# Kernel tuning notes

Hardware: AMD Instinct MI355X
Metric: run time of the kernel (lower is better)

The kernel has to match this reference:

```python
import jax, jax.numpy as jnp
import numpy as np

ALPHA = 0.2          # LeakyReLU negative slope
NEG_BIG = -9e15      # mask fill value from the original code
N, IN_F, OUT_F = 8192, 128, 64


def setup_inputs() -> dict:
    key = jax.random.key(0)
    k1, k2, k3, k4 = jax.random.split(key, 4)
    h = jax.random.normal(k1, (N, IN_F), dtype=jnp.float32)
    adj = jax.random.randint(k2, (N, N), 0, 2, dtype=jnp.int32)
    W = jax.random.normal(k3, (IN_F, OUT_F), dtype=jnp.float32) * 0.1
    a = jax.random.normal(k4, (2 * OUT_F, 1), dtype=jnp.float32) * 0.1
    return {"h": h, "adj": adj, "W": W, "a": a}


def reference(h, adj, W, a):
    # Wh: [N, F]
    Wh = h @ W
    # e_ij = leakyrelu([Wh_i ; Wh_j] . a) = leakyrelu(Wh_i.a1 + Wh_j.a2)
    # (identical math to the original NxNx2F concat, without materializing it)
    a1 = a[:OUT_F, 0]   # [F]
    a2 = a[OUT_F:, 0]   # [F]
    s1 = Wh @ a1        # [N]
    s2 = Wh @ a2        # [N]
    e = jax.nn.leaky_relu(s1[:, None] + s2[None, :], negative_slope=ALPHA)  # [N, N]
    e = jnp.where(adj > 0, e, jnp.float32(NEG_BIG))
    attention = jax.nn.softmax(e, axis=1)
    # dropout is identity at inference (training=False)
    h_prime = attention @ Wh  # [N, F]
    return jax.nn.elu(h_prime)  # concat=True -> elu
```

## Files before the change

### kernel.cpp

```cpp
#include <hip/hip_runtime.h>
#include <hip/hip_bf16.h>

#define N 8192
#define IN_F 128
#define OUT_F 64
#define LRELU_ALPHA 0.2f
#define CH 1024
#define NIT 8
#define PSTR 1040

typedef __attribute__((ext_vector_type(8))) short short8;
typedef __attribute__((ext_vector_type(4))) float float4v;
typedef __attribute__((ext_vector_type(4))) unsigned short ushortx4;

__device__ __forceinline__ unsigned short bf16_bits(float x) {
  unsigned u = __builtin_bit_cast(unsigned, x);
  u += 0x7fffu + ((u >> 16) & 1u);
  return (unsigned short)(u >> 16);
}

__global__ __launch_bounds__(256) void prep_kernel(
    const float* __restrict__ h, const float* __restrict__ W,
    const float* __restrict__ a, float* __restrict__ s1,
    float* __restrict__ s2, unsigned short* __restrict__ whT) {
  const int tid = threadIdx.x;
  const int row = blockIdx.x * 4 + (tid >> 6);
  const int k = tid & 63;
  const float* hr = h + row * IN_F;
  float acc = 0.f;
#pragma unroll 8
  for (int c = 0; c < IN_F; ++c) acc = fmaf(hr[c], W[c * OUT_F + k], acc);
  whT[(long)k * N + row] = bf16_bits(acc);
  float p1 = acc * a[k];
  float p2 = acc * a[OUT_F + k];
#pragma unroll
  for (int off = 32; off > 0; off >>= 1) {
    p1 += __shfl_xor(p1, off);
    p2 += __shfl_xor(p2, off);
  }
  if (k == 0) { s1[row] = p1; s2[row] = p2; }
}

__global__ __launch_bounds__(256) void repack_kernel(
    const unsigned short* __restrict__ whT, unsigned short* __restrict__ whF) {
  const int f = blockIdx.x * 256 + threadIdx.x;
  const int lane = f & 63, tt = (f >> 6) & 3, c = f >> 8;
  const int r16 = lane & 15, quad = lane >> 4;
  const short8 v = *(const short8*)(whT + (long)(tt * 16 + r16) * N + c * 32 + quad * 8);
  *(short8*)(whF + (long)f * 8) = v;
}

__device__ __forceinline__ void p_write(unsigned short* pr, int c, int4 av,
                                        float4 s2v, float s1w) {
  float e0 = s1w + s2v.x; e0 = fmaxf(e0, LRELU_ALPHA * e0);
  float e1 = s1w + s2v.y; e1 = fmaxf(e1, LRELU_ALPHA * e1);
  float e2 = s1w + s2v.z; e2 = fmaxf(e2, LRELU_ALPHA * e2);
  float e3 = s1w + s2v.w; e3 = fmaxf(e3, LRELU_ALPHA * e3);
  const float p0 = av.x > 0 ? __expf(e0) : 0.f;
  const float p1 = av.y > 0 ? __expf(e1) : 0.f;
  const float p2 = av.z > 0 ? __expf(e2) : 0.f;
  const float p3 = av.w > 0 ? __expf(e3) : 0.f;
  ushortx4 pk = {bf16_bits(p0), bf16_bits(p1), bf16_bits(p2), bf16_bits(p3)};
  *(ushortx4*)(pr + c) = pk;
}

__global__ __launch_bounds__(1024, 4) void gat_kernel(
    const int* __restrict__ adj, const float* __restrict__ s1,
    const float* __restrict__ s2, const unsigned short* __restrict__ whF,
    float* __restrict__ out) {
  __shared__ __align__(16) unsigned short pbuf[2][16][PSTR];
  const int tid = threadIdx.x;
  const int w = tid >> 6, L = tid & 63;
  const int r16 = L & 15, quad = L >> 4;
  const int row0 = blockIdx.x * 16;
  const long arow = (long)(row0 + w) * N;
  const float s1w = s1[row0 + w];

  float4v acc0 = {0.f, 0.f, 0.f, 0.f};
  float4v acc1 = {0.f, 0.f, 0.f, 0.f};
  float4v acc2 = {0.f, 0.f, 0.f, 0.f};
  float4v acc3 = {0.f, 0.f, 0.f, 0.f};
  float4v accD = {0.f, 0.f, 0.f, 0.f};
  const short ONE = (short)0x3F80;
  const short8 ones = {ONE, ONE, ONE, ONE, ONE, ONE, ONE, ONE};

  int4 ra[4];
  float4 rs[4];
#pragma unroll
  for (int k = 0; k < 4; ++k) {
    ra[k] = *(const int4*)(adj + arow + k * 256 + L * 4);
    rs[k] = *(const float4*)(s2 + k * 256 + L * 4);
  }
#pragma unroll
  for (int k = 0; k < 4; ++k)
    p_write(pbuf[0][w], k * 256 + L * 4, ra[k], rs[k], s1w);
#pragma unroll
  for (int k = 0; k < 4; ++k) {
    ra[k] = *(const int4*)(adj + arow + CH + k * 256 + L * 4);
    rs[k] = *(const float4*)(s2 + CH + k * 256 + L * 4);
  }
  __syncthreads();

  for (int it = 0; it < NIT; ++it) {
    const int b = it & 1;
    if (it < NIT - 1) {
      unsigned short* pr = pbuf[b ^ 1][w];
#pragma unroll
      for (int k = 0; k < 4; ++k)
        p_write(pr, k * 256 + L * 4, ra[k], rs[k], s1w);
      if (it < NIT - 2) {
        const long base = arow + (long)(it + 2) * CH + L * 4;
        const int sbase = (it + 2) * CH + L * 4;
#pragma unroll
        for (int k = 0; k < 4; ++k) {
          ra[k] = *(const int4*)(adj + base + k * 256);
          rs[k] = *(const float4*)(s2 + sbase + k * 256);
        }
      }
    }
#pragma unroll
    for (int sub = 0; sub < 2; ++sub) {
      const int lc = (sub * 16 + w) * 32;
      const short8 afrag = *(const short8*)(&pbuf[b][r16][lc + quad * 8]);
      const int c32 = it * 32 + sub * 16 + w;
      const unsigned short* bp = whF + ((long)c32 * 256 + L) * 8;
      const short8 b0 = *(const short8*)(bp);
      const short8 b1 = *(const short8*)(bp + 512);
      const short8 b2 = *(const short8*)(bp + 1024);
      const short8 b3 = *(const short8*)(bp + 1536);
      acc0 = __builtin_amdgcn_mfma_f32_16x16x32_bf16(afrag, b0, acc0, 0, 0, 0);
      acc1 = __builtin_amdgcn_mfma_f32_16x16x32_bf16(afrag, b1, acc1, 0, 0, 0);
      acc2 = __builtin_amdgcn_mfma_f32_16x16x32_bf16(afrag, b2, acc2, 0, 0, 0);
      acc3 = __builtin_amdgcn_mfma_f32_16x16x32_bf16(afrag, b3, acc3, 0, 0, 0);
      accD = __builtin_amdgcn_mfma_f32_16x16x32_bf16(afrag, ones, accD, 0, 0, 0);
    }
    __syncthreads();
  }

  float* M = (float*)pbuf;
  if (w >= 8) {
    float* S = M + (w - 8) * 1040;
#pragma unroll
    for (int reg = 0; reg < 4; ++reg) {
      const int r = quad * 4 + reg;
      S[r * 64 + 0 * 16 + r16] = acc0[reg];
      S[r * 64 + 1 * 16 + r16] = acc1[reg];
      S[r * 64 + 2 * 16 + r16] = acc2[reg];
      S[r * 64 + 3 * 16 + r16] = acc3[reg];
      if (r16 == 0) S[1024 + r] = accD[reg];
    }
  }
  __syncthreads();
  if (w < 8) {
    float* S = M + w * 1040;
#pragma unroll
    for (int reg = 0; reg < 4; ++reg) {
      const int r = quad * 4 + reg;
      S[r * 64 + 0 * 16 + r16] += acc0[reg];
      S[r * 64 + 1 * 16 + r16] += acc1[reg];
      S[r * 64 + 2 * 16 + r16] += acc2[reg];
      S[r * 64 + 3 * 16 + r16] += acc3[reg];
      if (r16 == 0) S[1024 + r] += accD[reg];
    }
  }
  __syncthreads();
  {
    const int r = tid >> 6, k = tid & 63;
    float Sv = 0.f, Lv = 0.f;
#pragma unroll
    for (int s = 0; s < 8; ++s) {
      Sv += M[s * 1040 + r * 64 + k];
      Lv += M[s * 1040 + 1024 + r];
    }
    const float v = Sv / Lv;
    out[(long)(row0 + r) * OUT_F + k] = v > 0.f ? v : expm1f(v);
  }
}

extern "C" void kernel_launch(void* const* d_in, const int* in_sizes, int n_in,
                              void* d_out, int out_size, void* d_ws, size_t ws_size,
                              hipStream_t stream) {
  const float* h = (const float*)d_in[0];
  const int* adj = (const int*)d_in[1];
  const float* W = (const float*)d_in[2];
  const float* a = (const float*)d_in[3];
  float* out = (float*)d_out;

  float* s1 = (float*)d_ws;
  float* s2 = s1 + N;
  unsigned short* whT = (unsigned short*)(s2 + N);
  unsigned short* whF = whT + (long)OUT_F * N;

  prep_kernel<<<N / 4, 256, 0, stream>>>(h, W, a, s1, s2, whT);
  repack_kernel<<<N * OUT_F / 8 / 256, 256, 0, stream>>>(whT, whF);
  gat_kernel<<<N / 16, 1024, 0, stream>>>(adj, s1, s2, whF, out);
}
```

Measured before the change: 397.6 us.

## Split columns across blocks with 64-row tiles and a separate merge kernel

Restructures the attention kernel so each block handles 64 rows and a quarter of the columns (split-K). Each whF B-fragment load is now reused across four row tiles instead of one. The row sum moves from an MFMA against a ones vector to a scalar accumulation plus wave shuffles. Partial numerators and denominators go to workspace, and a new merge kernel sums them and applies normalization and ELU. This cuts redundant global reads of Wh, but adds workspace traffic, an extra launch and higher register pressure from 16 accumulators.

```diff
diff --git a/kernel.cpp b/kernel.cpp
--- a/kernel.cpp
+++ b/kernel.cpp
@@ -5,11 +5,15 @@
 #define IN_F 128
 #define OUT_F 64
 #define LRELU_ALPHA 0.2f
-#define CH 1024
-#define NIT 8
-#define PSTR 1040
+#define SPLIT 4
+#define RPB 64
+#define CPB 2048
+#define WIN 512
+#define NWIN 4
+#define TSTR 129
 
 typedef __attribute__((ext_vector_type(8))) short short8;
+typedef __attribute__((ext_vector_type(4))) short short4v;
 typedef __attribute__((ext_vector_type(4))) float float4v;
 typedef __attribute__((ext_vector_type(4))) unsigned short ushortx4;
 
@@ -50,7 +54,7 @@
   *(short8*)(whF + (long)f * 8) = v;
 }
 
-__device__ __forceinline__ void p_write(unsigned short* pr, int c, int4 av,
+__device__ __forceinline__ float p_half(unsigned short* dst, int4 av,
                                         float4 s2v, float s1w) {
   float e0 = s1w + s2v.x; e0 = fmaxf(e0, LRELU_ALPHA * e0);
   float e1 = s1w + s2v.y; e1 = fmaxf(e1, LRELU_ALPHA * e1);
@@ -61,120 +65,154 @@
   const float p2 = av.z > 0 ? __expf(e2) : 0.f;
   const float p3 = av.w > 0 ? __expf(e3) : 0.f;
   ushortx4 pk = {bf16_bits(p0), bf16_bits(p1), bf16_bits(p2), bf16_bits(p3)};
-  *(ushortx4*)(pr + c) = pk;
-}
-
-__global__ __launch_bounds__(1024, 4) void gat_kernel(
+  *(ushortx4*)dst = pk;
+  return (p0 + p1) + (p2 + p3);
+}
+
+__global__ __launch_bounds__(512, 4) void gat_kernel(
     const int* __restrict__ adj, const float* __restrict__ s1,
     const float* __restrict__ s2, const unsigned short* __restrict__ whF,
-    float* __restrict__ out) {
-  __shared__ __align__(16) unsigned short pbuf[2][16][PSTR];
+    float* __restrict__ pacc, float* __restrict__ pl) {
+  __shared__ __align__(16) unsigned short ptile[RPB * TSTR * 4];
+  __shared__ __align__(16) float s2l[CPB];
   const int tid = threadIdx.x;
   const int w = tid >> 6, L = tid & 63;
   const int r16 = L & 15, quad = L >> 4;
-  const int row0 = blockIdx.x * 16;
-  const long arow = (long)(row0 + w) * N;
-  const float s1w = s1[row0 + w];
-
-  float4v acc0 = {0.f, 0.f, 0.f, 0.f};
-  float4v acc1 = {0.f, 0.f, 0.f, 0.f};
-  float4v acc2 = {0.f, 0.f, 0.f, 0.f};
-  float4v acc3 = {0.f, 0.f, 0.f, 0.f};
-  float4v accD = {0.f, 0.f, 0.f, 0.f};
-  const short ONE = (short)0x3F80;
-  const short8 ones = {ONE, ONE, ONE, ONE, ONE, ONE, ONE, ONE};
-
-  int4 ra[4];
-  float4 rs[4];
-#pragma unroll
-  for (int k = 0; k < 4; ++k) {
-    ra[k] = *(const int4*)(adj + arow + k * 256 + L * 4);
-    rs[k] = *(const float4*)(s2 + k * 256 + L * 4);
-  }
-#pragma unroll
-  for (int k = 0; k < 4; ++k)
-    p_write(pbuf[0][w], k * 256 + L * 4, ra[k], rs[k], s1w);
-#pragma unroll
-  for (int k = 0; k < 4; ++k) {
-    ra[k] = *(const int4*)(adj + arow + CH + k * 256 + L * 4);
-    rs[k] = *(const float4*)(s2 + CH + k * 256 + L * 4);
-  }
+  const int rb = blockIdx.x, cs = blockIdx.y;
+  const int row0 = rb * RPB;
+  const int colbase = cs * CPB;
+
+  *(float4*)(s2l + tid * 4) = *(const float4*)(s2 + colbase + tid * 4);
+
+  float s1r[8];
+#pragma unroll
+  for (int j = 0; j < 8; ++j) s1r[j] = s1[row0 + w * 8 + j];
+
+  float lsum[8] = {0.f, 0.f, 0.f, 0.f, 0.f, 0.f, 0.f, 0.f};
+  float4v acc[4][4];
+#pragma unroll
+  for (int rt = 0; rt < 4; ++rt)
+#pragma unroll
+    for (int dt = 0; dt < 4; ++dt) acc[rt][dt] = (float4v){0.f, 0.f, 0.f, 0.f};
+
   __syncthreads();
 
-  for (int it = 0; it < NIT; ++it) {
-    const int b = it & 1;
-    if (it < NIT - 1) {
-      unsigned short* pr = pbuf[b ^ 1][w];
-#pragma unroll
-      for (int k = 0; k < 4; ++k)
-        p_write(pr, k * 256 + L * 4, ra[k], rs[k], s1w);
-      if (it < NIT - 2) {
-        const long base = arow + (long)(it + 2) * CH + L * 4;
-        const int sbase = (it + 2) * CH + L * 4;
-#pragma unroll
-        for (int k = 0; k < 4; ++k) {
-          ra[k] = *(const int4*)(adj + base + k * 256);
-          rs[k] = *(const float4*)(s2 + sbase + k * 256);
-        }
+  for (int it = 0; it < NWIN; ++it) {
+    const int c0 = it * WIN + L * 4;
+    const float4 sva = *(const float4*)(s2l + c0);
+    const float4 svb = *(const float4*)(s2l + c0 + 256);
+#pragma unroll
+    for (int half = 0; half < 2; ++half) {
+      int4 ja[4], jb[4];
+#pragma unroll
+      for (int j2 = 0; j2 < 4; ++j2) {
+        const int r = half * 4 + j2;
+        const long arow = (long)(row0 + w * 8 + r) * N + colbase + c0;
+        ja[j2] = *(const int4*)(adj + arow);
+        jb[j2] = *(const int4*)(adj + arow + 256);
+      }
+#pragma unroll
+      for (int j2 = 0; j2 < 4; ++j2) {
+        const int r = half * 4 + j2;
+        unsigned short* rowp = ptile + (w * 8 + r) * TSTR * 4;
+        lsum[r] += p_half(rowp + L * 4, ja[j2], sva, s1r[r]);
+        lsum[r] += p_half(rowp + (64 + L) * 4, jb[j2], svb, s1r[r]);
       }
     }
-#pragma unroll
-    for (int sub = 0; sub < 2; ++sub) {
-      const int lc = (sub * 16 + w) * 32;
-      const short8 afrag = *(const short8*)(&pbuf[b][r16][lc + quad * 8]);
-      const int c32 = it * 32 + sub * 16 + w;
-      const unsigned short* bp = whF + ((long)c32 * 256 + L) * 8;
+    __syncthreads();
+#pragma unroll
+    for (int ci = 0; ci < 2; ++ci) {
+      const int c = w + ci * 8;
+      const unsigned short* bp =
+          whF + ((long)(cs * 64 + it * 16 + c) * 256 + L) * 8;
       const short8 b0 = *(const short8*)(bp);
       const short8 b1 = *(const short8*)(bp + 512);
       const short8 b2 = *(const short8*)(bp + 1024);
       const short8 b3 = *(const short8*)(bp + 1536);
-      acc0 = __builtin_amdgcn_mfma_f32_16x16x32_bf16(afrag, b0, acc0, 0, 0, 0);
-      acc1 = __builtin_amdgcn_mfma_f32_16x16x32_bf16(afrag, b1, acc1, 0, 0, 0);
-      acc2 = __builtin_amdgcn_mfma_f32_16x16x32_bf16(afrag, b2, acc2, 0, 0, 0);
-      acc3 = __builtin_amdgcn_mfma_f32_16x16x32_bf16(afrag, b3, acc3, 0, 0, 0);
-      accD = __builtin_amdgcn_mfma_f32_16x16x32_bf16(afrag, ones, accD, 0, 0, 0);
+#pragma unroll
+      for (int rt = 0; rt < 4; ++rt) {
+        const int g = (rt * 16 + r16) * TSTR + c * 8 + quad * 2;
+        const short4v alo = *(const short4v*)(ptile + g * 4);
+        const short4v ahi = *(const short4v*)(ptile + g * 4 + 4);
+        const short8 afrag =
+            __builtin_shufflevector(alo, ahi, 0, 1, 2, 3, 4, 5, 6, 7);
+        acc[rt][0] = __builtin_amdgcn_mfma_f32_16x16x32_bf16(afrag, b0, acc[rt][0], 0, 0, 0);
+        acc[rt][1] = __builtin_amdgcn_mfma_f32_16x16x32_bf16(afrag, b1, acc[rt][1], 0, 0, 0);
+        acc[rt][2] = __builtin_amdgcn_mfma_f32_16x16x32_bf16(afrag, b2, acc[rt][2], 0, 0, 0);
+        acc[rt][3] = __builtin_amdgcn_mfma_f32_16x16x32_bf16(afrag, b3, acc[rt][3], 0, 0, 0);
+      }
     }
     __syncthreads();
   }
 
-  float* M = (float*)pbuf;
-  if (w >= 8) {
-    float* S = M + (w - 8) * 1040;
-#pragma unroll
-    for (int reg = 0; reg < 4; ++reg) {
-      const int r = quad * 4 + reg;
-      S[r * 64 + 0 * 16 + r16] = acc0[reg];
-      S[r * 64 + 1 * 16 + r16] = acc1[reg];
-      S[r * 64 + 2 * 16 + r16] = acc2[reg];
-      S[r * 64 + 3 * 16 + r16] = acc3[reg];
-      if (r16 == 0) S[1024 + r] = accD[reg];
-    }
+#pragma unroll
+  for (int j = 0; j < 8; ++j) {
+    float v = lsum[j];
+#pragma unroll
+    for (int off = 1; off < 64; off <<= 1) v += __shfl_xor(v, off);
+    if (L == 0) pl[(long)cs * N + row0 + w * 8 + j] = v;
+  }
+
+  float* M = (float*)ptile;
+  if (w >= 4) {
+    float* S = M + (w - 4) * 4096;
+#pragma unroll
+    for (int rt = 0; rt < 4; ++rt)
+#pragma unroll
+      for (int dt = 0; dt < 4; ++dt)
+#pragma unroll
+        for (int reg = 0; reg < 4; ++reg)
+          S[(rt * 16 + quad * 4 + reg) * 64 + dt * 16 + r16] = acc[rt][dt][reg];
   }
   __syncthreads();
-  if (w < 8) {
-    float* S = M + w * 1040;
-#pragma unroll
-    for (int reg = 0; reg < 4; ++reg) {
-      const int r = quad * 4 + reg;
-      S[r * 64 + 0 * 16 + r16] += acc0[reg];
-      S[r * 64 + 1 * 16 + r16] += acc1[reg];
-      S[r * 64 + 2 * 16 + r16] += acc2[reg];
-      S[r * 64 + 3 * 16 + r16] += acc3[reg];
-      if (r16 == 0) S[1024 + r] += accD[reg];
-    }
+  if (w < 4) {
+    float* S = M + w * 4096;
+#pragma unroll
+    for (int rt = 0; rt < 4; ++rt)
+#pragma unroll
+      for (int dt = 0; dt < 4; ++dt)
+#pragma unroll
+        for (int reg = 0; reg < 4; ++reg)
+          S[(rt * 16 + quad * 4 + reg) * 64 + dt * 16 + r16] += acc[rt][dt][reg];
   }
   __syncthreads();
-  {
-    const int r = tid >> 6, k = tid & 63;
-    float Sv = 0.f, Lv = 0.f;
-#pragma unroll
-    for (int s = 0; s < 8; ++s) {
-      Sv += M[s * 1040 + r * 64 + k];
-      Lv += M[s * 1040 + 1024 + r];
-    }
-    const float v = Sv / Lv;
-    out[(long)(row0 + r) * OUT_F + k] = v > 0.f ? v : expm1f(v);
-  }
+#pragma unroll
+  for (int o = tid; o < 1024; o += 512) {
+    const int r = o >> 4, k4 = (o & 15) * 4;
+    float4 v0 = *(const float4*)(M + 0 * 4096 + r * 64 + k4);
+    const float4 v1 = *(const float4*)(M + 1 * 4096 + r * 64 + k4);
+    const float4 v2 = *(const float4*)(M + 2 * 4096 + r * 64 + k4);
+    const float4 v3 = *(const float4*)(M + 3 * 4096 + r * 64 + k4);
+    v0.x += v1.x + v2.x + v3.x;
+    v0.y += v1.y + v2.y + v3.y;
+    v0.z += v1.z + v2.z + v3.z;
+    v0.w += v1.w + v2.w + v3.w;
+    *(float4*)(pacc + ((long)cs * N + row0 + r) * OUT_F + k4) = v0;
+  }
+}
+
+__global__ __launch_bounds__(256) void merge_kernel(
+    const float* __restrict__ pacc, const float* __restrict__ pl,
+    float* __restrict__ out) {
+  const int idx = blockIdx.x * 256 + threadIdx.x;
+  const int r = idx >> 4;
+  const int k4 = (idx & 15) * 4;
+  float4 S = {0.f, 0.f, 0.f, 0.f};
+  float Lx = 0.f;
+#pragma unroll
+  for (int c = 0; c < SPLIT; ++c) {
+    const float4 p = *(const float4*)(pacc + ((long)c * N + r) * OUT_F + k4);
+    S.x += p.x; S.y += p.y; S.z += p.z; S.w += p.w;
+    Lx += pl[(long)c * N + r];
+  }
+  const float inv = 1.f / Lx;
+  float v[4] = {S.x * inv, S.y * inv, S.z * inv, S.w * inv};
+  float4 o;
+  o.x = v[0] > 0.f ? v[0] : expm1f(v[0]);
+  o.y = v[1] > 0.f ? v[1] : expm1f(v[1]);
+  o.z = v[2] > 0.f ? v[2] : expm1f(v[2]);
+  o.w = v[3] > 0.f ? v[3] : expm1f(v[3]);
+  *(float4*)(out + (long)r * OUT_F + k4) = o;
 }
 
 extern "C" void kernel_launch(void* const* d_in, const int* in_sizes, int n_in,
@@ -190,8 +228,11 @@
   float* s2 = s1 + N;
   unsigned short* whT = (unsigned short*)(s2 + N);
   unsigned short* whF = whT + (long)OUT_F * N;
+  float* pacc = (float*)(whF + (long)OUT_F * N);
+  float* pl = pacc + (long)SPLIT * N * OUT_F;
 
   prep_kernel<<<N / 4, 256, 0, stream>>>(h, W, a, s1, s2, whT);
   repack_kernel<<<N * OUT_F / 8 / 256, 256, 0, stream>>>(whT, whF);
-  gat_kernel<<<N / 16, 1024, 0, stream>>>(adj, s1, s2, whF, out);
-}
+  gat_kernel<<<dim3(N / RPB, SPLIT), 512, 0, stream>>>(adj, s1, s2, whF, pacc, pl);
+  merge_kernel<<<N * OUT_F / 4 / 256, 256, 0, stream>>>(pacc, pl, out);
+}
```

After: 416.8 us. 4.8% more time.
